# Kernel tuning notes

Hardware: AMD Instinct MI355X
Metric: run time of the kernel (lower is better)

## Reference

```python
import jax, jax.numpy as jnp
import numpy as np


def setup_inputs() -> dict:
    key = jax.random.key(0)
    ks = jax.random.split(key, 6)
    B, T, D, H = 2, 2048, 1024, 16
    dk = D // H
    s = 0.02
    return {
        "x": jax.random.normal(ks[0], (B, T, D), dtype=jnp.float32),
        "Wq": jax.random.normal(ks[1], (H, dk, dk), dtype=jnp.float32) * s,
        "Wk": jax.random.normal(ks[2], (H, dk, dk), dtype=jnp.float32) * s,
        "Wv": jax.random.normal(ks[3], (H, dk, dk), dtype=jnp.float32) * s,
        "Wp": jax.random.normal(ks[4], (D, D), dtype=jnp.float32) * s,
        "bp": jnp.zeros((D,), dtype=jnp.float32),
    }


def reference(x, Wq, Wk, Wv, Wp, bp):
    B, T, D = x.shape
    H, dk, _ = Wq.shape
    # split into heads: [B, H, T, dk]
    xh = x.reshape(B, T, H, dk).transpose(0, 2, 1, 3)
    # per-head torch Linear (y = x @ W^T), all heads at once
    q = jnp.einsum('bhtd,hkd->bhtk', xh, Wq)
    k = jnp.einsum('bhtd,hkd->bhtk', xh, Wk)
    v = jnp.einsum('bhtd,hkd->bhtk', xh, Wv)
    scale = 1.0 / jnp.sqrt(jnp.float32(dk))  # original divides by sqrt(C) with C == d_k
    scores = jnp.einsum('bhqd,bhkd->bhqk', q, k) * scale
    causal = jnp.tril(jnp.ones((T, T), dtype=bool))
    scores = jnp.where(causal[None, None], scores, -jnp.inf)
    attn = jax.nn.softmax(scores, axis=-1)
    out = jnp.einsum('bhqk,bhkd->bhqd', attn, v)  # [B,H,T,dk]
    out = out.transpose(0, 2, 1, 3).reshape(B, T, D)  # concat heads
    return out @ Wp.T + bp
```

## Files before the change

kernel.cpp:

```cpp
#include <hip/hip_runtime.h>
#include <math.h>

#define B_ 2
#define T_ 2048
#define D_ 1024
#define H_ 16
#define DK 64
#define BH_ (B_*H_)

typedef __attribute__((ext_vector_type(8))) short short8;
typedef __attribute__((ext_vector_type(4))) float fragC;

#define MFMA32(A,B,C) __builtin_amdgcn_mfma_f32_16x16x32_bf16((A),(B),(C),0,0,0)

#if defined(__HIP_DEVICE_COMPILE__) && __has_builtin(__builtin_amdgcn_exp2f)
#define EXP2 __builtin_amdgcn_exp2f
#else
#define EXP2 exp2f
#endif

__device__ __forceinline__ unsigned short f2bf(float x) {
    union { float f; unsigned u; } c; c.f = x;
    unsigned r = c.u + 0x7fff + ((c.u >> 16) & 1);
    return (unsigned short)(r >> 16);
}

__device__ __forceinline__ unsigned pack2bf(float a, float b) {
    return (unsigned)f2bf(a) | ((unsigned)f2bf(b) << 16);
}

__device__ __forceinline__ unsigned permpack(float a, float b) {
    union { float f; unsigned u; } ca, cb; ca.f = a; cb.f = b;
    return __builtin_amdgcn_perm(cb.u, ca.u, 0x07060302);
}

__device__ __forceinline__ float truncbf(float x) {
    union { float f; unsigned u; } c; c.f = x;
    c.u &= 0xffff0000u;
    return c.f;
}

__device__ __forceinline__ short8 packbf8(float4 a, float4 b) {
    union { short8 v; unsigned u[4]; } r;
    r.u[0] = pack2bf(a.x, a.y); r.u[1] = pack2bf(a.z, a.w);
    r.u[2] = pack2bf(b.x, b.y); r.u[3] = pack2bf(b.z, b.w);
    return r.v;
}

__device__ __forceinline__ void gload_lds16(const void* g, void* l) {
    __builtin_amdgcn_global_load_lds(
        (const __attribute__((address_space(1))) unsigned int*)g,
        (__attribute__((address_space(3))) unsigned int*)l, 16, 0, 0);
}

__global__ __launch_bounds__(256) void qkv_kernel(
    const float* __restrict__ x,
    const float* __restrict__ Wq, const float* __restrict__ Wk,
    const float* __restrict__ Wv, const float* __restrict__ Wp,
    unsigned short* __restrict__ Wb,
    unsigned short* __restrict__ q, unsigned short* __restrict__ k,
    unsigned short* __restrict__ vt)
{
    __shared__ unsigned short Wl[3*64*64];

    const int bh = blockIdx.x;
    const int b  = bh >> 4, h = bh & 15;
    const int t0 = blockIdx.y * 128;
    const int tid = threadIdx.x;
    const int wave = tid >> 6, lane = tid & 63;
    const int n = lane & 15, quad = lane >> 4;

    {
        const int L = bh + (blockIdx.y << 5);
        const float* src = Wp + (size_t)L*2048 + tid*8;
        float4 a = *(const float4*)src;
        float4 b2 = *(const float4*)(src + 4);
        *(uint4*)(Wb + (size_t)L*2048 + tid*8) =
            make_uint4(pack2bf(a.x, a.y), pack2bf(a.z, a.w),
                       pack2bf(b2.x, b2.y), pack2bf(b2.z, b2.w));
    }

    #pragma unroll
    for (int mat = 0; mat < 3; ++mat) {
        const float* ws = ((mat == 0) ? Wq : (mat == 1) ? Wk : Wv)
                          + (size_t)h * 4096;
        #pragma unroll
        for (int j = 0; j < 2; ++j) {
            const int e = (j*256 + tid) * 8;
            float4 a = *(const float4*)&ws[e];
            float4 b2 = *(const float4*)&ws[e + 4];
            *(uint4*)&Wl[mat*4096 + e] =
                make_uint4(pack2bf(a.x, a.y), pack2bf(a.z, a.w),
                           pack2bf(b2.x, b2.y), pack2bf(b2.z, b2.w));
        }
    }

    const int tw = t0 + wave*32;
    short8 xf[2][2];
    #pragma unroll
    for (int rt = 0; rt < 2; ++rt) {
        const float* xr = &x[((size_t)b*T_ + tw + rt*16 + n)*D_ + h*DK];
        float4 a0 = *(const float4*)&xr[quad*8];
        float4 a1 = *(const float4*)&xr[quad*8 + 4];
        xf[rt][0] = packbf8(a0, a1);
        float4 b0 = *(const float4*)&xr[32 + quad*8];
        float4 b1 = *(const float4*)&xr[32 + quad*8 + 4];
        xf[rt][1] = packbf8(b0, b1);
    }
    __syncthreads();

    const float qsc = 0.125f * 1.44269504088896340736f;
    const int tb0 = blockIdx.y*8 + wave*2;
    #pragma unroll
    for (int mat = 0; mat < 3; ++mat) {
        const int wbase = mat * 4096;
        #pragma unroll
        for (int ct = 0; ct < 4; ++ct) {
            short8 wf0 = *(const short8*)&Wl[wbase + (ct*16 + n)*64 + quad*8];
            short8 wf1 = *(const short8*)&Wl[wbase + (ct*16 + n)*64 + 32 + quad*8];
            if (mat < 2) {
                #pragma unroll
                for (int rt = 0; rt < 2; ++rt) {
                    fragC z = {0.f,0.f,0.f,0.f};
                    z = MFMA32(wf0, xf[rt][0], z);
                    z = MFMA32(wf1, xf[rt][1], z);
                    if (mat == 0) {
                        z[0] *= qsc; z[1] *= qsc; z[2] *= qsc; z[3] *= qsc;
                    }
                    unsigned short* dstg = (mat == 0) ? q : k;
                    unsigned short* dp = &dstg[((size_t)bh*128 + tb0 + rt)*1024
                                               + (ct*2 + (quad>>1))*128 + n*8 + (quad&1)*4];
                    *(uint2*)dp = make_uint2(pack2bf(z[0], z[1]), pack2bf(z[2], z[3]));
                }
            } else {
                uint4 pv4;
                {
                    fragC z = {0.f,0.f,0.f,0.f};
                    z = MFMA32(xf[0][0], wf0, z);
                    z = MFMA32(xf[0][1], wf1, z);
                    pv4.x = pack2bf(z[0], z[1]); pv4.y = pack2bf(z[2], z[3]);
                }
                {
                    fragC z = {0.f,0.f,0.f,0.f};
                    z = MFMA32(xf[1][0], wf0, z);
                    z = MFMA32(xf[1][1], wf1, z);
                    pv4.z = pack2bf(z[0], z[1]); pv4.w = pack2bf(z[2], z[3]);
                }
                const int ktv = tw >> 6, pv = (tw >> 5) & 1;
                unsigned short* dp = &vt[(size_t)bh*131072 + ktv*4096
                                         + ct*1024 + pv*512 + lane*8];
                *(uint4*)dp = pv4;
            }
        }
    }
}

__global__ __launch_bounds__(256, 2) void attn_kernel(
    const unsigned short* __restrict__ q, const unsigned short* __restrict__ k,
    const unsigned short* __restrict__ vt, unsigned short* __restrict__ aout)
{
    __shared__ fragC Os[4][4][4][64];
    __shared__ float Ls[4][4][16];

    const int id = blockIdx.x;
    const int xc = id & 7, p = id >> 3;
    const int jj = p & 3, s = p >> 2, g = s & 7, r = s >> 3;
    const int bh = xc*4 + jj;
    const int qt = (r == 0) ? 31 - g : (r == 1) ? g : (r == 2) ? 23 - g : 8 + g;

    const int b   = bh >> 4, h = bh & 15;
    const int tid = threadIdx.x;
    const int w = tid >> 6, lane = tid & 63;
    const int n = lane & 15, quad = lane >> 4;

    short8 qf[4][2];
    #pragma unroll
    for (int qc = 0; qc < 4; ++qc) {
        const unsigned short* qb = &q[((size_t)bh*128 + qt*4 + qc)*1024 + n*8];
        qf[qc][0] = *(const short8*)&qb[quad*128];
        qf[qc][1] = *(const short8*)&qb[(4 + quad)*128];
    }

    fragC o[4][4];
    #pragma unroll
    for (int qc = 0; qc < 4; ++qc)
        #pragma unroll
        for (int dt = 0; dt < 4; ++dt) o[qc][dt] = (fragC){0.f,0.f,0.f,0.f};
    float lsc[4] = {0.f, 0.f, 0.f, 0.f};

    const unsigned short* kg = &k[(size_t)bh*131072 + lane*8];
    const unsigned short* vg = &vt[(size_t)bh*131072 + lane*8];
    const int nt = qt + 1;

    short8 kf[4][2];
    short8 vv[4][2];

    int t = w;
    if (t < nt) {
        #pragma unroll
        for (int ct = 0; ct < 4; ++ct) {
            kf[ct][0] = *(const short8*)&kg[t*4096 + ct*1024];
            kf[ct][1] = *(const short8*)&kg[t*4096 + ct*1024 + 512];
        }
        #pragma unroll
        for (int dt = 0; dt < 4; ++dt) {
            vv[dt][0] = *(const short8*)&vg[t*4096 + dt*1024];
            vv[dt][1] = *(const short8*)&vg[t*4096 + dt*1024 + 512];
        }
    }

    for (; t < nt; t += 4) {
        const bool diag = (t == qt);
        #pragma unroll
        for (int qc = 0; qc < 4; ++qc) {
            fragC c[4];
            __builtin_amdgcn_s_setprio(1);
            #pragma unroll
            for (int ct = 0; ct < 4; ++ct) {
                fragC z = {0.f,0.f,0.f,0.f};
                z = MFMA32(kf[ct][0], qf[qc][0], z);
                z = MFMA32(kf[ct][1], qf[qc][1], z);
                c[ct] = z;
            }
            __builtin_amdgcn_s_setprio(0);

            if (qc == 3 && t + 4 < nt) {
                #pragma unroll
                for (int ct = 0; ct < 4; ++ct) {
                    kf[ct][0] = *(const short8*)&kg[(t+4)*4096 + ct*1024];
                    kf[ct][1] = *(const short8*)&kg[(t+4)*4096 + ct*1024 + 512];
                }
            }

            union { unsigned u[4]; short8 v; } pb[2];
            float ls = 0.f;
            #pragma unroll
            for (int ct = 0; ct < 4; ++ct) {
                float p0 = EXP2(c[ct][0]), p1 = EXP2(c[ct][1]);
                float p2 = EXP2(c[ct][2]), p3 = EXP2(c[ct][3]);
                if (diag) {
                    const int lim = (qc*16 + n) - (ct*16 + quad*4);
                    if (0 > lim) p0 = 0.f;
                    if (1 > lim) p1 = 0.f;
                    if (2 > lim) p2 = 0.f;
                    if (3 > lim) p3 = 0.f;
                }
                p0 = truncbf(p0); p1 = truncbf(p1);
                p2 = truncbf(p2); p3 = truncbf(p3);
                ls += (p0 + p1) + (p2 + p3);
                pb[ct >> 1].u[(ct & 1)*2]     = permpack(p0, p1);
                pb[ct >> 1].u[(ct & 1)*2 + 1] = permpack(p2, p3);
            }
            lsc[qc] += ls;

            __builtin_amdgcn_s_setprio(1);
            #pragma unroll
            for (int pv = 0; pv < 2; ++pv) {
                #pragma unroll
                for (int dt = 0; dt < 4; ++dt)
                    o[qc][dt] = MFMA32(vv[dt][pv], pb[pv].v, o[qc][dt]);
            }
            __builtin_amdgcn_s_setprio(0);
        }

        if (t + 4 < nt) {
            #pragma unroll
            for (int dt = 0; dt < 4; ++dt) {
                vv[dt][0] = *(const short8*)&vg[(t+4)*4096 + dt*1024];
                vv[dt][1] = *(const short8*)&vg[(t+4)*4096 + dt*1024 + 512];
            }
        }
    }

    #pragma unroll
    for (int qc = 0; qc < 4; ++qc) {
        lsc[qc] += __shfl_xor(lsc[qc], 16);
        lsc[qc] += __shfl_xor(lsc[qc], 32);
    }

    #pragma unroll
    for (int qc = 0; qc < 4; ++qc) {
        #pragma unroll
        for (int dt = 0; dt < 4; ++dt)
            Os[w][qc][dt][lane] = o[qc][dt];
        if (quad == 0) Ls[w][qc][n] = lsc[qc];
    }
    __syncthreads();

    const float lsum = Ls[0][w][n] + Ls[1][w][n] + Ls[2][w][n] + Ls[3][w][n];
    const float inv = 1.0f / lsum;
    const int q0 = qt*64 + w*16;
    unsigned short* dp = &aout[((size_t)b*T_ + q0 + n)*D_ + h*DK + quad*4];
    #pragma unroll
    for (int dt = 0; dt < 4; ++dt) {
        fragC sum = Os[0][w][dt][lane] + Os[1][w][dt][lane]
                  + Os[2][w][dt][lane] + Os[3][w][dt][lane];
        *(uint2*)(dp + dt*16) =
            make_uint2(pack2bf(sum[0]*inv, sum[1]*inv),
                       pack2bf(sum[2]*inv, sum[3]*inv));
    }
}

__global__ __launch_bounds__(256, 3) void proj_kernel(
    const unsigned short* __restrict__ A, const unsigned short* __restrict__ Wb,
    const float* __restrict__ bp, float* __restrict__ out)
{
    __shared__ unsigned short As[2][64*64];
    __shared__ unsigned short Bs[2][128*64];

    const int id = blockIdx.x;
    const int xcd = id & 7, idx = id >> 3;
    const int m0 = (xcd*8 + (idx & 7)) * 64;
    const int n0 = (idx >> 3) * 128;
    const int tid = threadIdx.x;
    const int wave = tid >> 6, lane = tid & 63;
    const int wm = wave & 1, wn = wave >> 1;
    const int n = lane & 15, quad = lane >> 4;

    const int arow = tid >> 3, acol = (tid & 7) * 8;
    const unsigned short* ag = &A [(size_t)(m0 + arow)*1024 + acol];
    const unsigned short* bg = &Wb[(size_t)(n0 + arow)*1024 + acol];

    fragC acc[2][4];
    #pragma unroll
    for (int i = 0; i < 2; ++i)
        #pragma unroll
        for (int j = 0; j < 4; ++j) acc[i][j] = (fragC){0.f,0.f,0.f,0.f};

    auto stage = [&](int bu, int kt) {
        #pragma unroll
        for (int i2 = 0; i2 < 2; ++i2)
            gload_lds16(ag + (size_t)i2*32*1024 + kt*64, &As[bu][i2*2048 + tid*8]);
        #pragma unroll
        for (int j2 = 0; j2 < 4; ++j2)
            gload_lds16(bg + (size_t)j2*32*1024 + kt*64, &Bs[bu][j2*2048 + tid*8]);
    };

    stage(0, 0);
    for (int kt = 0; kt < 16; ++kt) {
        __syncthreads();
        if (kt < 15) stage((kt + 1) & 1, kt + 1);
        const unsigned short* Ab = As[kt & 1];
        const unsigned short* Bb = Bs[kt & 1];
        #pragma unroll
        for (int kk = 0; kk < 2; ++kk) {
            short8 af[2], bf[4];
            #pragma unroll
            for (int i = 0; i < 2; ++i)
                af[i] = *(const short8*)&Ab[(wm*32 + i*16 + n)*64 + kk*32 + quad*8];
            #pragma unroll
            for (int j = 0; j < 4; ++j)
                bf[j] = *(const short8*)&Bb[(wn*64 + j*16 + n)*64 + kk*32 + quad*8];
            #pragma unroll
            for (int i = 0; i < 2; ++i)
                #pragma unroll
                for (int j = 0; j < 4; ++j)
                    acc[i][j] = MFMA32(af[i], bf[j], acc[i][j]);
        }
    }

    #pragma unroll
    for (int i = 0; i < 2; ++i) {
        #pragma unroll
        for (int r = 0; r < 4; ++r) {
            const int m = m0 + wm*32 + i*16 + quad*4 + r;
            #pragma unroll
            for (int j = 0; j < 4; ++j) {
                const int col = n0 + wn*64 + j*16 + n;
                out[(size_t)m*1024 + col] = acc[i][j][r] + bp[col];
            }
        }
    }
}

extern "C" void kernel_launch(void* const* d_in, const int* in_sizes, int n_in,
                              void* d_out, int out_size, void* d_ws, size_t ws_size,
                              hipStream_t stream)
{
    const float* x  = (const float*)d_in[0];
    const float* Wq = (const float*)d_in[1];
    const float* Wk = (const float*)d_in[2];
    const float* Wv = (const float*)d_in[3];
    const float* Wp = (const float*)d_in[4];
    const float* bp = (const float*)d_in[5];
    float* out = (float*)d_out;

    const size_t per = (size_t)BH_ * T_ * DK;
    unsigned short* qws   = (unsigned short*)d_ws;
    unsigned short* kws   = qws + per;
    unsigned short* vtws  = kws + per;
    unsigned short* aws   = vtws + per;
    unsigned short* wbws  = aws + per;

    qkv_kernel<<<dim3(BH_, T_/128), 256, 0, stream>>>(x, Wq, Wk, Wv, Wp, wbws,
                                                      qws, kws, vtws);
    attn_kernel<<<dim3(1024), 256, 0, stream>>>(qws, kws, vtws, aws);
    proj_kernel<<<dim3(512), 256, 0, stream>>>(aws, wbws, bp, out);
}
```

Before: 130.8 us.

## Split attention work by query rows per wave instead of key tiles

Each wave now owns 16 query rows and walks every key tile, where before each wave owned all 64 query rows and handled every fourth key tile. This removes the cross-wave LDS reduction of partial outputs and row sums, and cuts per-wave accumulator registers so occupancy can rise to 3 blocks per CU. In exchange every wave loads the full K/V stream (4x more global/L2 loads per block), and a per-iteration s_barrier is added to keep the waves in step so those loads hit cache.

```diff
diff --git a/kernel.cpp b/kernel.cpp
--- a/kernel.cpp
+++ b/kernel.cpp
@@ -155,13 +155,10 @@
     }
 }
 
-__global__ __launch_bounds__(256, 2) void attn_kernel(
+__global__ __launch_bounds__(256, 3) void attn_kernel(
     const unsigned short* __restrict__ q, const unsigned short* __restrict__ k,
     const unsigned short* __restrict__ vt, unsigned short* __restrict__ aout)
 {
-    __shared__ fragC Os[4][4][4][64];
-    __shared__ float Ls[4][4][16];
-
     const int id = blockIdx.x;
     const int xc = id & 7, p = id >> 3;
     const int jj = p & 3, s = p >> 2, g = s & 7, r = s >> 3;
@@ -173,20 +170,17 @@
     const int w = tid >> 6, lane = tid & 63;
     const int n = lane & 15, quad = lane >> 4;
 
-    short8 qf[4][2];
-    #pragma unroll
-    for (int qc = 0; qc < 4; ++qc) {
-        const unsigned short* qb = &q[((size_t)bh*128 + qt*4 + qc)*1024 + n*8];
-        qf[qc][0] = *(const short8*)&qb[quad*128];
-        qf[qc][1] = *(const short8*)&qb[(4 + quad)*128];
-    }
-
-    fragC o[4][4];
-    #pragma unroll
-    for (int qc = 0; qc < 4; ++qc)
-        #pragma unroll
-        for (int dt = 0; dt < 4; ++dt) o[qc][dt] = (fragC){0.f,0.f,0.f,0.f};
-    float lsc[4] = {0.f, 0.f, 0.f, 0.f};
+    short8 qf0, qf1;
+    {
+        const unsigned short* qb = &q[((size_t)bh*128 + qt*4 + w)*1024 + n*8];
+        qf0 = *(const short8*)&qb[quad*128];
+        qf1 = *(const short8*)&qb[(4 + quad)*128];
+    }
+
+    fragC o[4];
+    #pragma unroll
+    for (int dt = 0; dt < 4; ++dt) o[dt] = (fragC){0.f,0.f,0.f,0.f};
+    float lsc = 0.f;
 
     const unsigned short* kg = &k[(size_t)bh*131072 + lane*8];
     const unsigned short* vg = &vt[(size_t)bh*131072 + lane*8];
@@ -195,109 +189,90 @@
     short8 kf[4][2];
     short8 vv[4][2];
 
-    int t = w;
-    if (t < nt) {
+    #pragma unroll
+    for (int ct = 0; ct < 4; ++ct) {
+        kf[ct][0] = *(const short8*)&kg[ct*1024];
+        kf[ct][1] = *(const short8*)&kg[ct*1024 + 512];
+    }
+    #pragma unroll
+    for (int dt = 0; dt < 4; ++dt) {
+        vv[dt][0] = *(const short8*)&vg[dt*1024];
+        vv[dt][1] = *(const short8*)&vg[dt*1024 + 512];
+    }
+
+    for (int t = 0; t < nt; ++t) {
+        __builtin_amdgcn_s_barrier();
+        const bool diag = (t == qt);
+
+        fragC c[4];
+        __builtin_amdgcn_s_setprio(1);
         #pragma unroll
         for (int ct = 0; ct < 4; ++ct) {
-            kf[ct][0] = *(const short8*)&kg[t*4096 + ct*1024];
-            kf[ct][1] = *(const short8*)&kg[t*4096 + ct*1024 + 512];
-        }
-        #pragma unroll
-        for (int dt = 0; dt < 4; ++dt) {
-            vv[dt][0] = *(const short8*)&vg[t*4096 + dt*1024];
-            vv[dt][1] = *(const short8*)&vg[t*4096 + dt*1024 + 512];
-        }
-    }
-
-    for (; t < nt; t += 4) {
-        const bool diag = (t == qt);
-        #pragma unroll
-        for (int qc = 0; qc < 4; ++qc) {
-            fragC c[4];
-            __builtin_amdgcn_s_setprio(1);
+            fragC z = {0.f,0.f,0.f,0.f};
+            z = MFMA32(kf[ct][0], qf0, z);
+            z = MFMA32(kf[ct][1], qf1, z);
+            c[ct] = z;
+        }
+        __builtin_amdgcn_s_setprio(0);
+
+        if (t + 1 < nt) {
             #pragma unroll
             for (int ct = 0; ct < 4; ++ct) {
-                fragC z = {0.f,0.f,0.f,0.f};
-                z = MFMA32(kf[ct][0], qf[qc][0], z);
-                z = MFMA32(kf[ct][1], qf[qc][1], z);
-                c[ct] = z;
-            }
-            __builtin_amdgcn_s_setprio(0);
-
-            if (qc == 3 && t + 4 < nt) {
-                #pragma unroll
-                for (int ct = 0; ct < 4; ++ct) {
-                    kf[ct][0] = *(const short8*)&kg[(t+4)*4096 + ct*1024];
-                    kf[ct][1] = *(const short8*)&kg[(t+4)*4096 + ct*1024 + 512];
-                }
-            }
-
-            union { unsigned u[4]; short8 v; } pb[2];
-            float ls = 0.f;
-            #pragma unroll
-            for (int ct = 0; ct < 4; ++ct) {
-                float p0 = EXP2(c[ct][0]), p1 = EXP2(c[ct][1]);
-                float p2 = EXP2(c[ct][2]), p3 = EXP2(c[ct][3]);
-                if (diag) {
-                    const int lim = (qc*16 + n) - (ct*16 + quad*4);
-                    if (0 > lim) p0 = 0.f;
-                    if (1 > lim) p1 = 0.f;
-                    if (2 > lim) p2 = 0.f;
-                    if (3 > lim) p3 = 0.f;
-                }
-                p0 = truncbf(p0); p1 = truncbf(p1);
-                p2 = truncbf(p2); p3 = truncbf(p3);
-                ls += (p0 + p1) + (p2 + p3);
-                pb[ct >> 1].u[(ct & 1)*2]     = permpack(p0, p1);
-                pb[ct >> 1].u[(ct & 1)*2 + 1] = permpack(p2, p3);
-            }
-            lsc[qc] += ls;
-
-            __builtin_amdgcn_s_setprio(1);
-            #pragma unroll
-            for (int pv = 0; pv < 2; ++pv) {
-                #pragma unroll
-                for (int dt = 0; dt < 4; ++dt)
-                    o[qc][dt] = MFMA32(vv[dt][pv], pb[pv].v, o[qc][dt]);
-            }
-            __builtin_amdgcn_s_setprio(0);
-        }
-
-        if (t + 4 < nt) {
+                kf[ct][0] = *(const short8*)&kg[(t+1)*4096 + ct*1024];
+                kf[ct][1] = *(const short8*)&kg[(t+1)*4096 + ct*1024 + 512];
+            }
+        }
+
+        union { unsigned u[4]; short8 v; } pb[2];
+        float ls = 0.f;
+        #pragma unroll
+        for (int ct = 0; ct < 4; ++ct) {
+            float p0 = EXP2(c[ct][0]), p1 = EXP2(c[ct][1]);
+            float p2 = EXP2(c[ct][2]), p3 = EXP2(c[ct][3]);
+            if (diag) {
+                const int lim = (w*16 + n) - (ct*16 + quad*4);
+                if (0 > lim) p0 = 0.f;
+                if (1 > lim) p1 = 0.f;
+                if (2 > lim) p2 = 0.f;
+                if (3 > lim) p3 = 0.f;
+            }
+            p0 = truncbf(p0); p1 = truncbf(p1);
+            p2 = truncbf(p2); p3 = truncbf(p3);
+            ls += (p0 + p1) + (p2 + p3);
+            pb[ct >> 1].u[(ct & 1)*2]     = permpack(p0, p1);
+            pb[ct >> 1].u[(ct & 1)*2 + 1] = permpack(p2, p3);
+        }
+        lsc += ls;
+
+        __builtin_amdgcn_s_setprio(1);
+        #pragma unroll
+        for (int pv = 0; pv < 2; ++pv) {
+            #pragma unroll
+            for (int dt = 0; dt < 4; ++dt)
+                o[dt] = MFMA32(vv[dt][pv], pb[pv].v, o[dt]);
+        }
+        __builtin_amdgcn_s_setprio(0);
+
+        if (t + 1 < nt) {
             #pragma unroll
             for (int dt = 0; dt < 4; ++dt) {
-                vv[dt][0] = *(const short8*)&vg[(t+4)*4096 + dt*1024];
-                vv[dt][1] = *(const short8*)&vg[(t+4)*4096 + dt*1024 + 512];
-            }
-        }
-    }
-
-    #pragma unroll
-    for (int qc = 0; qc < 4; ++qc) {
-        lsc[qc] += __shfl_xor(lsc[qc], 16);
-        lsc[qc] += __shfl_xor(lsc[qc], 32);
-    }
-
-    #pragma unroll
-    for (int qc = 0; qc < 4; ++qc) {
-        #pragma unroll
-        for (int dt = 0; dt < 4; ++dt)
-            Os[w][qc][dt][lane] = o[qc][dt];
-        if (quad == 0) Ls[w][qc][n] = lsc[qc];
-    }
-    __syncthreads();
-
-    const float lsum = Ls[0][w][n] + Ls[1][w][n] + Ls[2][w][n] + Ls[3][w][n];
-    const float inv = 1.0f / lsum;
+                vv[dt][0] = *(const short8*)&vg[(t+1)*4096 + dt*1024];
+                vv[dt][1] = *(const short8*)&vg[(t+1)*4096 + dt*1024 + 512];
+            }
+        }
+    }
+
+    lsc += __shfl_xor(lsc, 16);
+    lsc += __shfl_xor(lsc, 32);
+    const float inv = 1.0f / lsc;
+
     const int q0 = qt*64 + w*16;
     unsigned short* dp = &aout[((size_t)b*T_ + q0 + n)*D_ + h*DK + quad*4];
     #pragma unroll
     for (int dt = 0; dt < 4; ++dt) {
-        fragC sum = Os[0][w][dt][lane] + Os[1][w][dt][lane]
-                  + Os[2][w][dt][lane] + Os[3][w][dt][lane];
         *(uint2*)(dp + dt*16) =
-            make_uint2(pack2bf(sum[0]*inv, sum[1]*inv),
-                       pack2bf(sum[2]*inv, sum[3]*inv));
+            make_uint2(pack2bf(o[dt][0]*inv, o[dt][1]*inv),
+                       pack2bf(o[dt][2]*inv, o[dt][3]*inv));
     }
 }
 
```

Result: slower. 138.0 us (+5.5%).

## Stage V tiles in LDS via direct loads to raise attention occupancy

Applied to the files above, without the earlier changes.

V tiles are no longer held in registers. Each wave streams them straight from global memory into its own LDS buffer with direct global-to-LDS loads and reads the fragments back just before the PV MFMAs. The epilogue reduction now goes one query chunk at a time through a much smaller LDS buffer, and the score tile is computed in two halves to cut live registers. Together these free VGPRs and LDS so launch bounds can go from 2 to 3 blocks per CU, at the cost of more LDS traffic, explicit waitcnt stalls on each tile and more barriers in the epilogue.

```diff
diff --git a/kernel.cpp b/kernel.cpp
--- a/kernel.cpp
+++ b/kernel.cpp
@@ -155,18 +155,19 @@
     }
 }
 
-__global__ __launch_bounds__(256, 2) void attn_kernel(
+__global__ __launch_bounds__(256, 3) void attn_kernel(
     const unsigned short* __restrict__ q, const unsigned short* __restrict__ k,
     const unsigned short* __restrict__ vt, unsigned short* __restrict__ aout)
 {
-    __shared__ fragC Os[4][4][4][64];
-    __shared__ float Ls[4][4][16];
+    __shared__ unsigned short Vs[4][4096];
+    __shared__ fragC Osr[4][4][64];
+    __shared__ float Lsr[4][16];
 
     const int id = blockIdx.x;
     const int xc = id & 7, p = id >> 3;
-    const int jj = p & 3, s = p >> 2, g = s & 7, r = s >> 3;
+    const int jj = p & 3, s = p >> 2, g = s & 7, r2 = s >> 3;
     const int bh = xc*4 + jj;
-    const int qt = (r == 0) ? 31 - g : (r == 1) ? g : (r == 2) ? 23 - g : 8 + g;
+    const int qt = (r2 == 0) ? 31 - g : (r2 == 1) ? g : (r2 == 2) ? 23 - g : 8 + g;
 
     const int b   = bh >> 4, h = bh & 15;
     const int tid = threadIdx.x;
@@ -188,41 +189,64 @@
         for (int dt = 0; dt < 4; ++dt) o[qc][dt] = (fragC){0.f,0.f,0.f,0.f};
     float lsc[4] = {0.f, 0.f, 0.f, 0.f};
 
-    const unsigned short* kg = &k[(size_t)bh*131072 + lane*8];
-    const unsigned short* vg = &vt[(size_t)bh*131072 + lane*8];
+    const unsigned short* kg  = &k[(size_t)bh*131072 + lane*8];
+    const unsigned short* vgl = &vt[(size_t)bh*131072 + lane*8];
+    unsigned short* vls = &Vs[w][0];
     const int nt = qt + 1;
 
     short8 kf[4][2];
-    short8 vv[4][2];
 
     int t = w;
     if (t < nt) {
+        #pragma unroll
+        for (int seg = 0; seg < 8; ++seg)
+            gload_lds16(vgl + (size_t)t*4096 + seg*512, vls + seg*512);
         #pragma unroll
         for (int ct = 0; ct < 4; ++ct) {
             kf[ct][0] = *(const short8*)&kg[t*4096 + ct*1024];
             kf[ct][1] = *(const short8*)&kg[t*4096 + ct*1024 + 512];
         }
-        #pragma unroll
-        for (int dt = 0; dt < 4; ++dt) {
-            vv[dt][0] = *(const short8*)&vg[t*4096 + dt*1024];
-            vv[dt][1] = *(const short8*)&vg[t*4096 + dt*1024 + 512];
-        }
     }
 
     for (; t < nt; t += 4) {
         const bool diag = (t == qt);
         #pragma unroll
         for (int qc = 0; qc < 4; ++qc) {
-            fragC c[4];
-            __builtin_amdgcn_s_setprio(1);
-            #pragma unroll
-            for (int ct = 0; ct < 4; ++ct) {
-                fragC z = {0.f,0.f,0.f,0.f};
-                z = MFMA32(kf[ct][0], qf[qc][0], z);
-                z = MFMA32(kf[ct][1], qf[qc][1], z);
-                c[ct] = z;
-            }
-            __builtin_amdgcn_s_setprio(0);
+            union { unsigned u[4]; short8 v; } pb[2];
+            float ls = 0.f;
+            #pragma unroll
+            for (int cp = 0; cp < 2; ++cp) {
+                fragC c[2];
+                __builtin_amdgcn_s_setprio(1);
+                #pragma unroll
+                for (int c2 = 0; c2 < 2; ++c2) {
+                    const int ct = cp*2 + c2;
+                    fragC z = {0.f,0.f,0.f,0.f};
+                    z = MFMA32(kf[ct][0], qf[qc][0], z);
+                    z = MFMA32(kf[ct][1], qf[qc][1], z);
+                    c[c2] = z;
+                }
+                __builtin_amdgcn_s_setprio(0);
+                #pragma unroll
+                for (int c2 = 0; c2 < 2; ++c2) {
+                    const int ct = cp*2 + c2;
+                    float p0 = EXP2(c[c2][0]), p1 = EXP2(c[c2][1]);
+                    float p2 = EXP2(c[c2][2]), p3 = EXP2(c[c2][3]);
+                    if (diag) {
+                        const int lim = (qc*16 + n) - (ct*16 + quad*4);
+                        if (0 > lim) p0 = 0.f;
+                        if (1 > lim) p1 = 0.f;
+                        if (2 > lim) p2 = 0.f;
+                        if (3 > lim) p3 = 0.f;
+                    }
+                    p0 = truncbf(p0); p1 = truncbf(p1);
+                    p2 = truncbf(p2); p3 = truncbf(p3);
+                    ls += (p0 + p1) + (p2 + p3);
+                    pb[cp].u[c2*2]     = permpack(p0, p1);
+                    pb[cp].u[c2*2 + 1] = permpack(p2, p3);
+                }
+            }
+            lsc[qc] += ls;
 
             if (qc == 3 && t + 4 < nt) {
                 #pragma unroll
@@ -232,43 +256,28 @@
                 }
             }
 
-            union { unsigned u[4]; short8 v; } pb[2];
-            float ls = 0.f;
-            #pragma unroll
-            for (int ct = 0; ct < 4; ++ct) {
-                float p0 = EXP2(c[ct][0]), p1 = EXP2(c[ct][1]);
-                float p2 = EXP2(c[ct][2]), p3 = EXP2(c[ct][3]);
-                if (diag) {
-                    const int lim = (qc*16 + n) - (ct*16 + quad*4);
-                    if (0 > lim) p0 = 0.f;
-                    if (1 > lim) p1 = 0.f;
-                    if (2 > lim) p2 = 0.f;
-                    if (3 > lim) p3 = 0.f;
-                }
-                p0 = truncbf(p0); p1 = truncbf(p1);
-                p2 = truncbf(p2); p3 = truncbf(p3);
-                ls += (p0 + p1) + (p2 + p3);
-                pb[ct >> 1].u[(ct & 1)*2]     = permpack(p0, p1);
-                pb[ct >> 1].u[(ct & 1)*2 + 1] = permpack(p2, p3);
-            }
-            lsc[qc] += ls;
+            if (qc == 0) {
+                asm volatile("s_waitcnt vmcnt(0)" ::: "memory");
+                __builtin_amdgcn_sched_barrier(0);
+            }
 
             __builtin_amdgcn_s_setprio(1);
             #pragma unroll
             for (int pv = 0; pv < 2; ++pv) {
                 #pragma unroll
-                for (int dt = 0; dt < 4; ++dt)
-                    o[qc][dt] = MFMA32(vv[dt][pv], pb[pv].v, o[qc][dt]);
+                for (int dt = 0; dt < 4; ++dt) {
+                    short8 vf = *(const short8*)&vls[dt*1024 + pv*512 + lane*8];
+                    o[qc][dt] = MFMA32(vf, pb[pv].v, o[qc][dt]);
+                }
             }
             __builtin_amdgcn_s_setprio(0);
         }
 
         if (t + 4 < nt) {
-            #pragma unroll
-            for (int dt = 0; dt < 4; ++dt) {
-                vv[dt][0] = *(const short8*)&vg[(t+4)*4096 + dt*1024];
-                vv[dt][1] = *(const short8*)&vg[(t+4)*4096 + dt*1024 + 512];
-            }
+            asm volatile("s_waitcnt lgkmcnt(0)" ::: "memory");
+            #pragma unroll
+            for (int seg = 0; seg < 8; ++seg)
+                gload_lds16(vgl + (size_t)(t+4)*4096 + seg*512, vls + seg*512);
         }
     }
 
@@ -279,25 +288,27 @@
     }
 
     #pragma unroll
-    for (int qc = 0; qc < 4; ++qc) {
+    for (int rr = 0; rr < 4; ++rr) {
+        __syncthreads();
         #pragma unroll
         for (int dt = 0; dt < 4; ++dt)
-            Os[w][qc][dt][lane] = o[qc][dt];
-        if (quad == 0) Ls[w][qc][n] = lsc[qc];
-    }
-    __syncthreads();
-
-    const float lsum = Ls[0][w][n] + Ls[1][w][n] + Ls[2][w][n] + Ls[3][w][n];
-    const float inv = 1.0f / lsum;
-    const int q0 = qt*64 + w*16;
-    unsigned short* dp = &aout[((size_t)b*T_ + q0 + n)*D_ + h*DK + quad*4];
-    #pragma unroll
-    for (int dt = 0; dt < 4; ++dt) {
-        fragC sum = Os[0][w][dt][lane] + Os[1][w][dt][lane]
-                  + Os[2][w][dt][lane] + Os[3][w][dt][lane];
-        *(uint2*)(dp + dt*16) =
-            make_uint2(pack2bf(sum[0]*inv, sum[1]*inv),
-                       pack2bf(sum[2]*inv, sum[3]*inv));
+            Osr[w][dt][lane] = o[rr][dt];
+        if (quad == 0) Lsr[w][n] = lsc[rr];
+        __syncthreads();
+        if (w == rr) {
+            const float lsum = Lsr[0][n] + Lsr[1][n] + Lsr[2][n] + Lsr[3][n];
+            const float inv = 1.0f / lsum;
+            const int q0 = qt*64 + rr*16;
+            unsigned short* dp = &aout[((size_t)b*T_ + q0 + n)*D_ + h*DK + quad*4];
+            #pragma unroll
+            for (int dt = 0; dt < 4; ++dt) {
+                fragC sum = Osr[0][dt][lane] + Osr[1][dt][lane]
+                          + Osr[2][dt][lane] + Osr[3][dt][lane];
+                *(uint2*)(dp + dt*16) =
+                    make_uint2(pack2bf(sum[0]*inv, sum[1]*inv),
+                               pack2bf(sum[2]*inv, sum[3]*inv));
+            }
+        }
     }
 }
 
```

After: 202.5 us. +54.8%, slower.

## Double-buffer K fragments two tiles ahead and interleave QK MFMA with softmax

Applied to the files above, without the earlier changes.

The attention loop keeps two K register buffers (A/B) and unrolls the tile loop by two. Each buffer is refilled with the tile eight steps ahead, so K loads have a full tile of work to hide their latency. The QK^T MFMAs are also split into pairs of column tiles, each followed by its exp/mask/pack work, so matrix and vector work can interleave. This adds 16 more VGPRs for the second K buffer, which under launch_bounds(256,2) may cause spills or lower occupancy.

```diff
diff --git a/kernel.cpp b/kernel.cpp
--- a/kernel.cpp
+++ b/kernel.cpp
@@ -164,9 +164,9 @@
 
     const int id = blockIdx.x;
     const int xc = id & 7, p = id >> 3;
-    const int jj = p & 3, s = p >> 2, g = s & 7, r = s >> 3;
+    const int jj = p & 3, s = p >> 2, g = s & 7, r2 = s >> 3;
     const int bh = xc*4 + jj;
-    const int qt = (r == 0) ? 31 - g : (r == 1) ? g : (r == 2) ? 23 - g : 8 + g;
+    const int qt = (r2 == 0) ? 31 - g : (r2 == 1) ? g : (r2 == 2) ? 23 - g : 8 + g;
 
     const int b   = bh >> 4, h = bh & 15;
     const int tid = threadIdx.x;
@@ -192,66 +192,57 @@
     const unsigned short* vg = &vt[(size_t)bh*131072 + lane*8];
     const int nt = qt + 1;
 
-    short8 kf[4][2];
+    short8 kfA[4][2], kfB[4][2];
     short8 vv[4][2];
 
-    int t = w;
-    if (t < nt) {
-        #pragma unroll
-        for (int ct = 0; ct < 4; ++ct) {
-            kf[ct][0] = *(const short8*)&kg[t*4096 + ct*1024];
-            kf[ct][1] = *(const short8*)&kg[t*4096 + ct*1024 + 512];
-        }
-        #pragma unroll
-        for (int dt = 0; dt < 4; ++dt) {
-            vv[dt][0] = *(const short8*)&vg[t*4096 + dt*1024];
-            vv[dt][1] = *(const short8*)&vg[t*4096 + dt*1024 + 512];
-        }
-    }
-
-    for (; t < nt; t += 4) {
-        const bool diag = (t == qt);
+    auto tile_body = [&](short8 (&kf)[4][2], short8 (&kfn)[4][2],
+                         int tt, bool pre, int tn) {
+        const bool diag = (tt == qt);
         #pragma unroll
         for (int qc = 0; qc < 4; ++qc) {
-            fragC c[4];
-            __builtin_amdgcn_s_setprio(1);
-            #pragma unroll
-            for (int ct = 0; ct < 4; ++ct) {
-                fragC z = {0.f,0.f,0.f,0.f};
-                z = MFMA32(kf[ct][0], qf[qc][0], z);
-                z = MFMA32(kf[ct][1], qf[qc][1], z);
-                c[ct] = z;
-            }
-            __builtin_amdgcn_s_setprio(0);
-
-            if (qc == 3 && t + 4 < nt) {
-                #pragma unroll
-                for (int ct = 0; ct < 4; ++ct) {
-                    kf[ct][0] = *(const short8*)&kg[(t+4)*4096 + ct*1024];
-                    kf[ct][1] = *(const short8*)&kg[(t+4)*4096 + ct*1024 + 512];
-                }
-            }
-
             union { unsigned u[4]; short8 v; } pb[2];
             float ls = 0.f;
             #pragma unroll
-            for (int ct = 0; ct < 4; ++ct) {
-                float p0 = EXP2(c[ct][0]), p1 = EXP2(c[ct][1]);
-                float p2 = EXP2(c[ct][2]), p3 = EXP2(c[ct][3]);
-                if (diag) {
-                    const int lim = (qc*16 + n) - (ct*16 + quad*4);
-                    if (0 > lim) p0 = 0.f;
-                    if (1 > lim) p1 = 0.f;
-                    if (2 > lim) p2 = 0.f;
-                    if (3 > lim) p3 = 0.f;
-                }
-                p0 = truncbf(p0); p1 = truncbf(p1);
-                p2 = truncbf(p2); p3 = truncbf(p3);
-                ls += (p0 + p1) + (p2 + p3);
-                pb[ct >> 1].u[(ct & 1)*2]     = permpack(p0, p1);
-                pb[ct >> 1].u[(ct & 1)*2 + 1] = permpack(p2, p3);
+            for (int cp = 0; cp < 2; ++cp) {
+                fragC c[2];
+                __builtin_amdgcn_s_setprio(1);
+                #pragma unroll
+                for (int c2 = 0; c2 < 2; ++c2) {
+                    const int ct = cp*2 + c2;
+                    fragC z = {0.f,0.f,0.f,0.f};
+                    z = MFMA32(kf[ct][0], qf[qc][0], z);
+                    z = MFMA32(kf[ct][1], qf[qc][1], z);
+                    c[c2] = z;
+                }
+                __builtin_amdgcn_s_setprio(0);
+                #pragma unroll
+                for (int c2 = 0; c2 < 2; ++c2) {
+                    const int ct = cp*2 + c2;
+                    float p0 = EXP2(c[c2][0]), p1 = EXP2(c[c2][1]);
+                    float p2 = EXP2(c[c2][2]), p3 = EXP2(c[c2][3]);
+                    if (diag) {
+                        const int lim = (qc*16 + n) - (ct*16 + quad*4);
+                        if (0 > lim) p0 = 0.f;
+                        if (1 > lim) p1 = 0.f;
+                        if (2 > lim) p2 = 0.f;
+                        if (3 > lim) p3 = 0.f;
+                    }
+                    p0 = truncbf(p0); p1 = truncbf(p1);
+                    p2 = truncbf(p2); p3 = truncbf(p3);
+                    ls += (p0 + p1) + (p2 + p3);
+                    pb[cp].u[c2*2]     = permpack(p0, p1);
+                    pb[cp].u[c2*2 + 1] = permpack(p2, p3);
+                }
             }
             lsc[qc] += ls;
+
+            if (qc == 3 && pre) {
+                #pragma unroll
+                for (int ct = 0; ct < 4; ++ct) {
+                    kfn[ct][0] = *(const short8*)&kg[(size_t)tn*4096 + ct*1024];
+                    kfn[ct][1] = *(const short8*)&kg[(size_t)tn*4096 + ct*1024 + 512];
+                }
+            }
 
             __builtin_amdgcn_s_setprio(1);
             #pragma unroll
@@ -263,14 +254,42 @@
             __builtin_amdgcn_s_setprio(0);
         }
 
-        if (t + 4 < nt) {
+        if (tt + 4 < nt) {
             #pragma unroll
             for (int dt = 0; dt < 4; ++dt) {
-                vv[dt][0] = *(const short8*)&vg[(t+4)*4096 + dt*1024];
-                vv[dt][1] = *(const short8*)&vg[(t+4)*4096 + dt*1024 + 512];
-            }
-        }
-    }
+                vv[dt][0] = *(const short8*)&vg[(size_t)(tt+4)*4096 + dt*1024];
+                vv[dt][1] = *(const short8*)&vg[(size_t)(tt+4)*4096 + dt*1024 + 512];
+            }
+        }
+    };
+
+    int t = w;
+    int cnt = (nt > w) ? ((nt - w + 3) >> 2) : 0;
+    if (cnt > 0) {
+        #pragma unroll
+        for (int dt = 0; dt < 4; ++dt) {
+            vv[dt][0] = *(const short8*)&vg[(size_t)t*4096 + dt*1024];
+            vv[dt][1] = *(const short8*)&vg[(size_t)t*4096 + dt*1024 + 512];
+        }
+        #pragma unroll
+        for (int ct = 0; ct < 4; ++ct) {
+            kfA[ct][0] = *(const short8*)&kg[(size_t)t*4096 + ct*1024];
+            kfA[ct][1] = *(const short8*)&kg[(size_t)t*4096 + ct*1024 + 512];
+        }
+        if (cnt > 1) {
+            #pragma unroll
+            for (int ct = 0; ct < 4; ++ct) {
+                kfB[ct][0] = *(const short8*)&kg[(size_t)(t+4)*4096 + ct*1024];
+                kfB[ct][1] = *(const short8*)&kg[(size_t)(t+4)*4096 + ct*1024 + 512];
+            }
+        }
+    }
+    while (cnt >= 2) {
+        tile_body(kfA, kfA, t,     cnt > 2, t + 8);
+        tile_body(kfB, kfB, t + 4, cnt > 3, t + 12);
+        t += 8; cnt -= 2;
+    }
+    if (cnt == 1) tile_body(kfA, kfA, t, false, 0);
 
     #pragma unroll
     for (int qc = 0; qc < 4; ++qc) {
```

Result: slower. 221.6 us (+69.4%).
